# Kernel tuning notes

Hardware: AMD Instinct MI355X
Metric: run time of the kernel (lower is better)

The kernel has to match this reference:

```python
import jax, jax.numpy as jnp
import numpy as np

N = 100000
D = 128
E = 1600000
NEG_SLOPE = 0.2


def gatv2_layer(x, src, dst, Wl, Wr, att, b):
    # GATv2Conv (heads=1, eval mode): lin_l -> source/message feats, lin_r -> target feats
    xl = x @ Wl                      # [N, D]
    xr = x @ Wr                      # [N, D]
    # per-edge score: a^T LeakyReLU(x_l[src] + x_r[dst])
    z = jax.nn.leaky_relu(xl[src] + xr[dst], NEG_SLOPE)  # [E, D]
    e = z @ att                      # [E]
    # segment softmax over incoming edges of each dst node
    m = jax.ops.segment_max(e, dst, num_segments=N)      # [N]
    ex = jnp.exp(e - m[dst])
    s = jax.ops.segment_sum(ex, dst, num_segments=N)     # [N]
    alpha = ex / (s[dst] + 1e-16)                        # [E]
    # weighted scatter-aggregate of source messages
    out = jax.ops.segment_sum(alpha[:, None] * xl[src], dst, num_segments=N)
    return out + b


def setup_inputs() -> dict:
    key = jax.random.key(0)
    ks = jax.random.split(key, 6)
    scale = 1.0 / np.sqrt(D)
    x = jax.random.normal(ks[0], (N, D), dtype=jnp.float32)
    edge_index = jax.random.randint(ks[1], (2, E), 0, N, dtype=jnp.int64)
    Wl = jax.random.normal(ks[2], (3, D, D), dtype=jnp.float32) * scale
    Wr = jax.random.normal(ks[3], (3, D, D), dtype=jnp.float32) * scale
    att = jax.random.normal(ks[4], (3, D), dtype=jnp.float32) * scale
    b = jax.random.normal(ks[5], (3, D), dtype=jnp.float32) * 0.01
    return {"x": x, "Wl": Wl, "Wr": Wr, "att": att, "b": b, "edge_index": edge_index}


def reference(x, Wl, Wr, att, b, edge_index):
    src, dst = edge_index[0], edge_index[1]
    h = gatv2_layer(x, src, dst, Wl[0], Wr[0], att[0], b[0])
    h = jax.nn.relu(h)
    h = gatv2_layer(h, src, dst, Wl[1], Wr[1], att[1], b[1])
    h = jax.nn.relu(h)
    h = gatv2_layer(h, src, dst, Wl[2], Wr[2], att[2], b[2])
    return h
```

## Files before the change

### kernel.cpp

```cpp
#include <hip/hip_runtime.h>
#include <math.h>

#define DD 128
#define NEG 0.2f

typedef short short8 __attribute__((ext_vector_type(8)));
typedef float f32x4 __attribute__((ext_vector_type(4)));
typedef float f32x2 __attribute__((ext_vector_type(2)));
typedef _Float16 h2v __attribute__((ext_vector_type(2)));

__device__ __forceinline__ unsigned short f2bf(float f) {
    unsigned u = __float_as_uint(f);
    return (unsigned short)((u + 0x7fffu + ((u >> 16) & 1u)) >> 16);
}
__device__ __forceinline__ float bf2f(unsigned short h) {
    return __uint_as_float(((unsigned)h) << 16);
}

#if __has_builtin(__builtin_amdgcn_exp2f)
#define EXP2F(x) __builtin_amdgcn_exp2f(x)
#else
#define EXP2F(x) exp2f(x)
#endif

__device__ void excl_scan_1024(int* sh, int* aux) {
    __syncthreads();
    int t = threadIdx.x;
    int base = t * 4;
    int a0 = sh[base], a1 = sh[base + 1], a2 = sh[base + 2], a3 = sh[base + 3];
    int s = a0 + a1 + a2 + a3;
    aux[t] = s;
    __syncthreads();
    for (int off = 1; off < 256; off <<= 1) {
        int v = (t >= off) ? aux[t - off] : 0;
        __syncthreads();
        aux[t] += v;
        __syncthreads();
    }
    int excl = aux[t] - s;
    sh[base] = excl;
    sh[base + 1] = excl + a0;
    sh[base + 2] = excl + a0 + a1;
    sh[base + 3] = excl + a0 + a1 + a2;
    __syncthreads();
}

__global__ __launch_bounds__(256) void k_histC(const int* __restrict__ dst,
                                               int* __restrict__ histC, int E, int CB) {
    __shared__ int h[1024];
    int t = threadIdx.x;
    for (int j = t; j < 1024; j += 256) h[j] = 0;
    __syncthreads();
    int stride = gridDim.x * 256;
    for (int i = blockIdx.x * 256 + t; i < E; i += stride)
        atomicAdd(&h[dst[i] >> 7], 1);
    __syncthreads();
    for (int j = t; j < CB; j += 256)
        if (h[j]) atomicAdd(&histC[j], h[j]);
}

__global__ __launch_bounds__(256) void k_scanC2(const int* __restrict__ histC,
                                                int* __restrict__ baseC,
                                                int* __restrict__ cursorC, int CB) {
    __shared__ int sh[1024];
    __shared__ int aux[256];
    int t = threadIdx.x;
    for (int j = t; j < 1024; j += 256) sh[j] = (j < CB) ? histC[j] : 0;
    excl_scan_1024(sh, aux);
    for (int j = t; j <= CB; j += 256) {
        baseC[j] = sh[j];
        if (j < CB) cursorC[j] = sh[j];
    }
}

#define CHUNK 8192
__global__ __launch_bounds__(256) void k_part3(const int* __restrict__ srcI,
                                               const int* __restrict__ dstI,
                                               int* __restrict__ cursorC,
                                               uint2* __restrict__ part,
                                               int E, int CB) {
    __shared__ int sh[1024];
    __shared__ int aux[256];
    __shared__ int resBase[1024];
    __shared__ int cur[1024];
    __shared__ uint2 stage[CHUNK];
    int t = threadIdx.x;
    int c0 = blockIdx.x * CHUNK;
    int cnt = E - c0; if (cnt > CHUNK) cnt = CHUNK;

    for (int j = t; j < 1024; j += 256) sh[j] = 0;
    __syncthreads();
    for (int i = t; i < cnt; i += 256)
        atomicAdd(&sh[dstI[c0 + i] >> 7], 1);
    __syncthreads();
    for (int j = t; j < CB; j += 256) {
        int c = sh[j];
        resBase[j] = c ? atomicAdd(&cursorC[j], c) : 0;
    }
    excl_scan_1024(sh, aux);
    for (int j = t; j < 1024; j += 256) cur[j] = sh[j];
    __syncthreads();
    for (int i = t; i < cnt; i += 256) {
        unsigned s = (unsigned)srcI[c0 + i];
        unsigned d = (unsigned)dstI[c0 + i];
        int b = (int)(d >> 7);
        int pos = atomicAdd(&cur[b], 1);
        stage[pos].x = s;
        stage[pos].y = d;
    }
    __syncthreads();
    for (int i = t; i < cnt; i += 256) {
        uint2 v = stage[i];
        int b = (int)(v.y >> 7);
        part[resBase[b] + (i - sh[b])] = v;
    }
}

__global__ __launch_bounds__(256) void k_part4(const uint2* __restrict__ part,
                                               const int* __restrict__ baseC,
                                               int* __restrict__ srcs,
                                               int* __restrict__ row_ptr,
                                               int N) {
    __shared__ int hist[128];
    __shared__ int incl[128];
    __shared__ int cur[128];
    __shared__ unsigned srcS[8192];
    int b = blockIdx.x;
    int t = threadIdx.x;
    int base = baseC[b];
    int cnt = baseC[b + 1] - base;
    int node0 = b << 7;

    if (t < 128) hist[t] = 0;
    __syncthreads();
    for (int i = t; i < cnt; i += 256)
        atomicAdd(&hist[part[base + i].y & 127], 1);
    __syncthreads();
    if (t < 128) incl[t] = hist[t];
    __syncthreads();
    for (int off = 1; off < 128; off <<= 1) {
        int v = 0;
        if (t < 128 && t >= off) v = incl[t - off];
        __syncthreads();
        if (t < 128) incl[t] += v;
        __syncthreads();
    }
    if (t < 128) cur[t] = incl[t] - hist[t];
    __syncthreads();
    for (int i = t; i < cnt; i += 256) {
        uint2 e = part[base + i];
        int r = atomicAdd(&cur[e.y & 127], 1);
        if (r < 8192) srcS[r] = e.x;
    }
    __syncthreads();
    for (int i = t; i < cnt; i += 256)
        srcs[base + i] = (int)srcS[i];
    int nodes = N - node0; if (nodes > 128) nodes = 128;
    if (t < nodes) row_ptr[node0 + t + 1] = base + incl[t];
    if (b == 0 && t == 0) row_ptr[0] = 0;
}

__global__ void k_castx(const float* __restrict__ x, unsigned short* __restrict__ hi,
                        unsigned short* __restrict__ lo, int n) {
    int i = (blockIdx.x * blockDim.x + threadIdx.x) * 4;
    if (i >= n) return;
    float4 v = *(const float4*)(x + i);
    unsigned short h[4], l[4];
    float f[4] = {v.x, v.y, v.z, v.w};
#pragma unroll
    for (int j = 0; j < 4; j++) {
        h[j] = f2bf(f[j]);
        l[j] = f2bf(f[j] - bf2f(h[j]));
    }
    *(uint2*)(hi + i) = *(uint2*)h;
    *(uint2*)(lo + i) = *(uint2*)l;
}

__global__ void k_castw(const float* __restrict__ Wl, const float* __restrict__ Wr,
                        unsigned short* __restrict__ Wth, unsigned short* __restrict__ Wtl) {
    int idx = blockIdx.x * blockDim.x + threadIdx.x;
    if (idx >= 3 * 256 * 128) return;
    int L = idx >> 15;
    int rem = idx & 32767;
    int nn = rem >> 7;
    int k = rem & 127;
    float v = (nn < 128) ? Wl[L * 16384 + k * 128 + nn]
                         : Wr[L * 16384 + k * 128 + (nn - 128)];
    unsigned short h = f2bf(v);
    Wth[idx] = h;
    Wtl[idx] = f2bf(v - bf2f(h));
}

__global__ __launch_bounds__(256) void k_gemm(const unsigned short* __restrict__ Ahi,
                                              const unsigned short* __restrict__ Alo,
                                              const unsigned short* __restrict__ Wth,
                                              const unsigned short* __restrict__ Wtl,
                                              _Float16* __restrict__ xl, _Float16* __restrict__ xr,
                                              int M, int L) {
    __shared__ unsigned short sA[2][128][40];
    __shared__ unsigned short sB[2][128][40];
    int t = threadIdx.x;
    int lane = t & 63;
    int l15 = lane & 15;
    int quad = lane >> 4;
    int wave = t >> 6;
    int wm = wave & 1;
    int wn = wave >> 1;
    int r0 = blockIdx.x * 128;
    const unsigned short* WthL = Wth + ((size_t)L * 256 + blockIdx.y * 128) * 128;
    const unsigned short* WtlL = Wtl + ((size_t)L * 256 + blockIdx.y * 128) * 128;

    f32x4 acc[4][4] = {};

    for (int kc = 0; kc < 4; kc++) {
        int k0 = kc * 32;
        if (kc) __syncthreads();
#pragma unroll
        for (int i = 0; i < 2; i++) {
            int s = t + i * 256;
            int row = s >> 2;
            int kq = (s & 3) * 8;
            int gr = r0 + row; gr = gr < M ? gr : M - 1;
            uint2 va0 = *(const uint2*)(Ahi + (size_t)gr * DD + k0 + kq);
            uint2 va1 = *(const uint2*)(Ahi + (size_t)gr * DD + k0 + kq + 4);
            *(uint2*)&sA[0][row][kq] = va0;
            *(uint2*)&sA[0][row][kq + 4] = va1;
            uint2 vb0 = *(const uint2*)(Alo + (size_t)gr * DD + k0 + kq);
            uint2 vb1 = *(const uint2*)(Alo + (size_t)gr * DD + k0 + kq + 4);
            *(uint2*)&sA[1][row][kq] = vb0;
            *(uint2*)&sA[1][row][kq + 4] = vb1;
            uint2 wa0 = *(const uint2*)(WthL + (size_t)row * DD + k0 + kq);
            uint2 wa1 = *(const uint2*)(WthL + (size_t)row * DD + k0 + kq + 4);
            *(uint2*)&sB[0][row][kq] = wa0;
            *(uint2*)&sB[0][row][kq + 4] = wa1;
            uint2 wb0 = *(const uint2*)(WtlL + (size_t)row * DD + k0 + kq);
            uint2 wb1 = *(const uint2*)(WtlL + (size_t)row * DD + k0 + kq + 4);
            *(uint2*)&sB[1][row][kq] = wb0;
            *(uint2*)&sB[1][row][kq + 4] = wb1;
        }
        __syncthreads();

        union F8 { short8 v; uint2 u[2]; };
        F8 ah[4], al[4], bh[4], bl[4];
#pragma unroll
        for (int mt = 0; mt < 4; mt++) {
            const unsigned short* p = &sA[0][wm * 64 + mt * 16 + l15][quad * 8];
            ah[mt].u[0] = *(const uint2*)p; ah[mt].u[1] = *(const uint2*)(p + 4);
            const unsigned short* q = &sA[1][wm * 64 + mt * 16 + l15][quad * 8];
            al[mt].u[0] = *(const uint2*)q; al[mt].u[1] = *(const uint2*)(q + 4);
        }
#pragma unroll
        for (int nt = 0; nt < 4; nt++) {
            const unsigned short* p = &sB[0][wn * 64 + nt * 16 + l15][quad * 8];
            bh[nt].u[0] = *(const uint2*)p; bh[nt].u[1] = *(const uint2*)(p + 4);
            const unsigned short* q = &sB[1][wn * 64 + nt * 16 + l15][quad * 8];
            bl[nt].u[0] = *(const uint2*)q; bl[nt].u[1] = *(const uint2*)(q + 4);
        }
#pragma unroll
        for (int mt = 0; mt < 4; mt++)
#pragma unroll
            for (int nt = 0; nt < 4; nt++) {
                acc[mt][nt] = __builtin_amdgcn_mfma_f32_16x16x32_bf16(ah[mt].v, bh[nt].v, acc[mt][nt], 0, 0, 0);
                acc[mt][nt] = __builtin_amdgcn_mfma_f32_16x16x32_bf16(al[mt].v, bh[nt].v, acc[mt][nt], 0, 0, 0);
                acc[mt][nt] = __builtin_amdgcn_mfma_f32_16x16x32_bf16(ah[mt].v, bl[nt].v, acc[mt][nt], 0, 0, 0);
            }
    }

    _Float16* C = blockIdx.y ? xr : xl;
#pragma unroll
    for (int mt = 0; mt < 4; mt++)
#pragma unroll
        for (int r = 0; r < 4; r++) {
            int row = r0 + wm * 64 + mt * 16 + quad * 4 + r;
            if (row < M) {
#pragma unroll
                for (int nt = 0; nt < 4; nt++)
                    C[(size_t)row * DD + wn * 64 + nt * 16 + l15] = (_Float16)acc[mt][nt][r];
            }
        }
}

__global__ __launch_bounds__(256) void k_attn(const _Float16* __restrict__ xl,
                                              const _Float16* __restrict__ xr,
                                              const int* __restrict__ row_ptr,
                                              const int* __restrict__ srcs,
                                              const float* __restrict__ att,
                                              const float* __restrict__ bias,
                                              float* __restrict__ outF,
                                              unsigned short* __restrict__ outHi,
                                              unsigned short* __restrict__ outLo,
                                              int n, int mode) {
    int d = (blockIdx.x * blockDim.x + threadIdx.x) >> 6;
    if (d >= n) return;
    int l = threadIdx.x & 63;
    int l15 = l & 15;
    int g = l >> 4;

    union Q { uint4 q; h2v h[4]; };
    const float LOG2E = 1.44269504088896f;

    h2v at[4], xrh[4];
    {
        float4 a0 = *(const float4*)(att + l15 * 8);
        float4 a1 = *(const float4*)(att + l15 * 8 + 4);
        at[0] = h2v{(_Float16)(a0.x * LOG2E), (_Float16)(a0.y * LOG2E)};
        at[1] = h2v{(_Float16)(a0.z * LOG2E), (_Float16)(a0.w * LOG2E)};
        at[2] = h2v{(_Float16)(a1.x * LOG2E), (_Float16)(a1.y * LOG2E)};
        at[3] = h2v{(_Float16)(a1.z * LOG2E), (_Float16)(a1.w * LOG2E)};
        Q hr; hr.q = *(const uint4*)(xr + (size_t)d * DD + l15 * 8);
#pragma unroll
        for (int j = 0; j < 4; j++) xrh[j] = hr.h[j];
    }
    const _Float16 cneg = (_Float16)NEG;

    int beg = row_ptr[d], end = row_ptr[d + 1];
    float lse = 0.f;
    float av[8] = {};

    int i0 = beg + g, i1 = beg + 4 + g;
    bool v0 = i0 < end, v1 = i1 < end;
    int s0 = (end > beg) ? srcs[v0 ? i0 : beg] : 0;
    int s1 = (end > beg) ? srcs[v1 ? i1 : beg] : 0;

    const _Float16* xlp = xl + l15 * 8;

    for (int i = beg; i < end; i += 8) {
        Q h0, h1;
        h0.q = *(const uint4*)(xlp + (size_t)s0 * DD);
        h1.q = *(const uint4*)(xlp + (size_t)s1 * DD);
        int n0 = i + 8 + g, n1 = i + 12 + g;
        bool nv0 = n0 < end, nv1 = n1 < end;
        int t0 = srcs[nv0 ? n0 : beg];
        int t1 = srcs[nv1 ? n1 : beg];

        float p0 = 0.f, p1 = 0.f;
#pragma unroll
        for (int j = 0; j < 4; j++) {
            h2v z0 = h0.h[j] + xrh[j];
            h2v zl0 = __builtin_elementwise_max(z0, z0 * cneg);
            p0 = __builtin_amdgcn_fdot2(zl0, at[j], p0, false);
            h2v z1 = h1.h[j] + xrh[j];
            h2v zl1 = __builtin_elementwise_max(z1, z1 * cneg);
            p1 = __builtin_amdgcn_fdot2(zl1, at[j], p1, false);
        }
        p0 += __shfl_xor(p0, 1, 64);  p1 += __shfl_xor(p1, 1, 64);
        p0 += __shfl_xor(p0, 2, 64);  p1 += __shfl_xor(p1, 2, 64);
        p0 += __shfl_xor(p0, 4, 64);  p1 += __shfl_xor(p1, 4, 64);
        p0 += __shfl_xor(p0, 8, 64);  p1 += __shfl_xor(p1, 8, 64);
        p0 = fminf(fmaxf(p0, -86.f), 86.f);
        p1 = fminf(fmaxf(p1, -86.f), 86.f);
        float w0 = v0 ? EXP2F(p0) : 0.f;
        float w1 = v1 ? EXP2F(p1) : 0.f;
        lse += w0 + w1;
#pragma unroll
        for (int j = 0; j < 4; j++) {
            av[2 * j]     += (float)h0.h[j][0] * w0;
            av[2 * j + 1] += (float)h0.h[j][1] * w0;
            av[2 * j]     += (float)h1.h[j][0] * w1;
            av[2 * j + 1] += (float)h1.h[j][1] * w1;
        }
        s0 = t0; s1 = t1; v0 = nv0; v1 = nv1;
    }

    lse += __shfl_xor(lse, 16, 64);
    lse += __shfl_xor(lse, 32, 64);
#pragma unroll
    for (int j = 0; j < 8; j++) {
        av[j] += __shfl_xor(av[j], 16, 64);
        av[j] += __shfl_xor(av[j], 32, 64);
    }

    if (l < 16) {
        float inv = (end > beg) ? 1.0f / lse : 0.f;
        float o[8];
        float4 b0 = *(const float4*)(bias + l15 * 8);
        float4 b1 = *(const float4*)(bias + l15 * 8 + 4);
        float bv[8] = {b0.x, b0.y, b0.z, b0.w, b1.x, b1.y, b1.z, b1.w};
#pragma unroll
        for (int j = 0; j < 8; j++) o[j] = av[j] * inv + bv[j];
        if (mode) {
            union U8 { unsigned short s[8]; uint4 q; };
            U8 hh, ll;
#pragma unroll
            for (int j = 0; j < 8; j++) {
                float v = fmaxf(o[j], 0.f);
                hh.s[j] = f2bf(v);
                ll.s[j] = f2bf(v - bf2f(hh.s[j]));
            }
            *(uint4*)(outHi + (size_t)d * DD + l15 * 8) = hh.q;
            *(uint4*)(outLo + (size_t)d * DD + l15 * 8) = ll.q;
        } else {
            float4 o0 = {o[0], o[1], o[2], o[3]};
            float4 o1 = {o[4], o[5], o[6], o[7]};
            float* op = outF + (size_t)d * DD + l15 * 8;
            *(float4*)op = o0;
            *(float4*)(op + 4) = o1;
        }
    }
}

extern "C" void kernel_launch(void* const* d_in, const int* in_sizes, int n_in,
                              void* d_out, int out_size, void* d_ws, size_t ws_size,
                              hipStream_t stream) {
    const float* x    = (const float*)d_in[0];
    const float* Wl   = (const float*)d_in[1];
    const float* Wr   = (const float*)d_in[2];
    const float* att  = (const float*)d_in[3];
    const float* bias = (const float*)d_in[4];
    const int*   ei   = (const int*)d_in[5];

    int N = in_sizes[0] / DD;
    int E = in_sizes[5] / 2;
    const int* srcI = ei;
    const int* dstI = ei + E;
    float* out = (float*)d_out;
    int CB = (N + 127) >> 7;

    char* ws = (char*)d_ws;
    size_t off = 0;
    auto alloc = [&](size_t bytes) -> void* {
        void* p = ws + off;
        off += (bytes + 255) & ~(size_t)255;
        return p;
    };
    _Float16*       xl   = (_Float16*)alloc((size_t)N * DD * 2);
    _Float16*       xr   = (_Float16*)alloc((size_t)N * DD * 2);
    unsigned short* Ahi  = (unsigned short*)alloc((size_t)N * DD * 2);
    unsigned short* Alo  = (unsigned short*)alloc((size_t)N * DD * 2);
    unsigned short* Wth  = (unsigned short*)alloc((size_t)3 * 256 * 128 * 2);
    unsigned short* Wtl  = (unsigned short*)alloc((size_t)3 * 256 * 128 * 2);
    uint2* part    = (uint2*)alloc((size_t)E * 8);
    int*   srcs    = (int*)alloc((size_t)E * 4);
    int*   row_ptr = (int*)alloc((size_t)(N + 1) * 4);
    int*   histC   = (int*)alloc((size_t)(CB + 1) * 4);
    int*   baseC   = (int*)alloc((size_t)(CB + 1) * 4);
    int*   cursorC = (int*)alloc((size_t)(CB + 1) * 4);

    const int tb = 256;
    (void)hipMemsetAsync(histC, 0, (size_t)CB * 4, stream);
    k_histC<<<256, 256, 0, stream>>>(dstI, histC, E, CB);
    k_scanC2<<<1, 256, 0, stream>>>(histC, baseC, cursorC, CB);
    k_part3<<<(E + CHUNK - 1) / CHUNK, 256, 0, stream>>>(srcI, dstI, cursorC, part, E, CB);
    k_part4<<<CB, 256, 0, stream>>>(part, baseC, srcs, row_ptr, N);

    k_castw<<<(3 * 256 * 128 + tb - 1) / tb, tb, 0, stream>>>(Wl, Wr, Wth, Wtl);
    k_castx<<<((size_t)N * DD / 4 + tb - 1) / tb, tb, 0, stream>>>(x, Ahi, Alo, N * DD);

    int gX = (N + 127) / 128;
    for (int L = 0; L < 3; ++L) {
        k_gemm<<<dim3(gX, 2), 256, 0, stream>>>(Ahi, Alo, Wth, Wtl, xl, xr, N, L);
        k_attn<<<((size_t)N * 64 + tb - 1) / tb, tb, 0, stream>>>(
            xl, xr, row_ptr, srcs, att + (size_t)L * DD, bias + (size_t)L * DD,
            out, Ahi, Alo, N, (L < 2) ? 1 : 0);
    }
}
```

Before: 515.4 us.

## Assign one node per 16-lane group and sort nodes by degree for balance

The attention kernel used to give each node a full 64-lane wavefront, with four 16-lane groups splitting that node's edges and a cross-group reduction at the end. Now each 16-lane group owns its own destination node. Nodes are bucketed by in-degree through a histogram, scan and scatter, so the four nodes in a wave have similar edge counts and lanes sit idle less. This removes the cross-group shuffles and quarters the grid, at the cost of three small preprocessing kernels and an indirect node lookup that makes output writes scattered.

```diff
diff --git a/kernel.cpp b/kernel.cpp
--- a/kernel.cpp
+++ b/kernel.cpp
@@ -158,6 +158,41 @@
     int nodes = N - node0; if (nodes > 128) nodes = 128;
     if (t < nodes) row_ptr[node0 + t + 1] = base + incl[t];
     if (b == 0 && t == 0) row_ptr[0] = 0;
+}
+
+__global__ __launch_bounds__(256) void k_deghist(const int* __restrict__ row_ptr,
+                                                 int* __restrict__ histD, int N) {
+    int d = blockIdx.x * 256 + threadIdx.x;
+    if (d >= N) return;
+    int deg = row_ptr[d + 1] - row_ptr[d];
+    int c = deg < 127 ? deg : 127;
+    atomicAdd(&histD[c], 1);
+}
+
+__global__ __launch_bounds__(128) void k_degscan(const int* __restrict__ histD,
+                                                 int* __restrict__ cursorD) {
+    __shared__ int sh[128];
+    int t = threadIdx.x;
+    int v0 = histD[t];
+    sh[t] = v0;
+    __syncthreads();
+    for (int off = 1; off < 128; off <<= 1) {
+        int v = (t >= off) ? sh[t - off] : 0;
+        __syncthreads();
+        sh[t] += v;
+        __syncthreads();
+    }
+    cursorD[t] = sh[t] - v0;
+}
+
+__global__ __launch_bounds__(256) void k_degscatter(const int* __restrict__ row_ptr,
+                                                    int* __restrict__ cursorD,
+                                                    int* __restrict__ order, int N) {
+    int d = blockIdx.x * 256 + threadIdx.x;
+    if (d >= N) return;
+    int deg = row_ptr[d + 1] - row_ptr[d];
+    int c = deg < 127 ? deg : 127;
+    order[atomicAdd(&cursorD[c], 1)] = d;
 }
 
 __global__ void k_castx(const float* __restrict__ x, unsigned short* __restrict__ hi,
@@ -284,17 +319,20 @@
                                               const _Float16* __restrict__ xr,
                                               const int* __restrict__ row_ptr,
                                               const int* __restrict__ srcs,
+                                              const int* __restrict__ order,
                                               const float* __restrict__ att,
                                               const float* __restrict__ bias,
                                               float* __restrict__ outF,
                                               unsigned short* __restrict__ outHi,
                                               unsigned short* __restrict__ outLo,
                                               int n, int mode) {
-    int d = (blockIdx.x * blockDim.x + threadIdx.x) >> 6;
-    if (d >= n) return;
+    int wid = (blockIdx.x * blockDim.x + threadIdx.x) >> 6;
     int l = threadIdx.x & 63;
     int l15 = l & 15;
     int g = l >> 4;
+    int idx = wid * 4 + g;
+    bool act = idx < n;
+    int d = act ? order[idx] : 0;
 
     union Q { uint4 q; h2v h[4]; };
     const float LOG2E = 1.44269504088896f;
@@ -313,25 +351,33 @@
     }
     const _Float16 cneg = (_Float16)NEG;
 
-    int beg = row_ptr[d], end = row_ptr[d + 1];
+    int beg = act ? row_ptr[d] : 0;
+    int end = act ? row_ptr[d + 1] : 0;
+    int cnt = end - beg;
+
+    int mc = cnt;
+    mc = max(mc, __shfl_xor(mc, 16, 64));
+    mc = max(mc, __shfl_xor(mc, 32, 64));
+    int iters = (mc + 1) >> 1;
+
     float lse = 0.f;
     float av[8] = {};
 
-    int i0 = beg + g, i1 = beg + 4 + g;
+    int i0 = beg, i1 = beg + 1;
     bool v0 = i0 < end, v1 = i1 < end;
-    int s0 = (end > beg) ? srcs[v0 ? i0 : beg] : 0;
-    int s1 = (end > beg) ? srcs[v1 ? i1 : beg] : 0;
+    int s0 = v0 ? srcs[i0] : 0;
+    int s1 = v1 ? srcs[i1] : 0;
 
     const _Float16* xlp = xl + l15 * 8;
 
-    for (int i = beg; i < end; i += 8) {
+    for (int it = 0; it < iters; ++it) {
         Q h0, h1;
         h0.q = *(const uint4*)(xlp + (size_t)s0 * DD);
         h1.q = *(const uint4*)(xlp + (size_t)s1 * DD);
-        int n0 = i + 8 + g, n1 = i + 12 + g;
+        int n0 = i0 + 2, n1 = i1 + 2;
         bool nv0 = n0 < end, nv1 = n1 < end;
-        int t0 = srcs[nv0 ? n0 : beg];
-        int t1 = srcs[nv1 ? n1 : beg];
+        int t0 = nv0 ? srcs[n0] : 0;
+        int t1 = nv1 ? srcs[n1] : 0;
 
         float p0 = 0.f, p1 = 0.f;
 #pragma unroll
@@ -359,19 +405,11 @@
             av[2 * j]     += (float)h1.h[j][0] * w1;
             av[2 * j + 1] += (float)h1.h[j][1] * w1;
         }
-        s0 = t0; s1 = t1; v0 = nv0; v1 = nv1;
-    }
-
-    lse += __shfl_xor(lse, 16, 64);
-    lse += __shfl_xor(lse, 32, 64);
-#pragma unroll
-    for (int j = 0; j < 8; j++) {
-        av[j] += __shfl_xor(av[j], 16, 64);
-        av[j] += __shfl_xor(av[j], 32, 64);
-    }
-
-    if (l < 16) {
-        float inv = (end > beg) ? 1.0f / lse : 0.f;
+        i0 = n0; i1 = n1; v0 = nv0; v1 = nv1; s0 = t0; s1 = t1;
+    }
+
+    if (act) {
+        float inv = (cnt > 0) ? 1.0f / lse : 0.f;
         float o[8];
         float4 b0 = *(const float4*)(bias + l15 * 8);
         float4 b1 = *(const float4*)(bias + l15 * 8 + 4);
@@ -432,16 +470,23 @@
     uint2* part    = (uint2*)alloc((size_t)E * 8);
     int*   srcs    = (int*)alloc((size_t)E * 4);
     int*   row_ptr = (int*)alloc((size_t)(N + 1) * 4);
+    int*   order   = (int*)alloc((size_t)N * 4);
     int*   histC   = (int*)alloc((size_t)(CB + 1) * 4);
     int*   baseC   = (int*)alloc((size_t)(CB + 1) * 4);
     int*   cursorC = (int*)alloc((size_t)(CB + 1) * 4);
+    int*   histD   = (int*)alloc(128 * 4);
+    int*   cursorD = (int*)alloc(128 * 4);
 
     const int tb = 256;
     (void)hipMemsetAsync(histC, 0, (size_t)CB * 4, stream);
+    (void)hipMemsetAsync(histD, 0, 128 * 4, stream);
     k_histC<<<256, 256, 0, stream>>>(dstI, histC, E, CB);
     k_scanC2<<<1, 256, 0, stream>>>(histC, baseC, cursorC, CB);
     k_part3<<<(E + CHUNK - 1) / CHUNK, 256, 0, stream>>>(srcI, dstI, cursorC, part, E, CB);
     k_part4<<<CB, 256, 0, stream>>>(part, baseC, srcs, row_ptr, N);
+    k_deghist<<<(N + 255) / 256, 256, 0, stream>>>(row_ptr, histD, N);
+    k_degscan<<<1, 128, 0, stream>>>(histD, cursorD);
+    k_degscatter<<<(N + 255) / 256, 256, 0, stream>>>(row_ptr, cursorD, order, N);
 
     k_castw<<<(3 * 256 * 128 + tb - 1) / tb, tb, 0, stream>>>(Wl, Wr, Wth, Wtl);
     k_castx<<<((size_t)N * DD / 4 + tb - 1) / tb, tb, 0, stream>>>(x, Ahi, Alo, N * DD);
@@ -449,8 +494,8 @@
     int gX = (N + 127) / 128;
     for (int L = 0; L < 3; ++L) {
         k_gemm<<<dim3(gX, 2), 256, 0, stream>>>(Ahi, Alo, Wth, Wtl, xl, xr, N, L);
-        k_attn<<<((size_t)N * 64 + tb - 1) / tb, tb, 0, stream>>>(
-            xl, xr, row_ptr, srcs, att + (size_t)L * DD, bias + (size_t)L * DD,
+        k_attn<<<((size_t)N * 16 + tb - 1) / tb, tb, 0, stream>>>(
+            xl, xr, row_ptr, srcs, order, att + (size_t)L * DD, bias + (size_t)L * DD,
             out, Ahi, Alo, N, (L < 2) ? 1 : 0);
     }
 }
```

New measurement: 1.012 ms. 96.4% more time.
